# Performance work log

Measured on AMD Instinct MI355X. Metric: run time of the kernel, lower is better.

Reference implementation:

```python
import jax, jax.numpy as jnp
import numpy as np

B, T, D = 32, 1024, 768
H = 768          # GRU hidden size
INNER = 512      # fc output size
NOUT = 39        # out_proj outputs (13 classes x 3 ACCDOA coords)


def setup_inputs() -> dict:
    key = jax.random.key(0)
    ks = jax.random.split(key, 16)
    s_in = 1.0 / np.sqrt(H)
    inp = {
        "features": jax.random.normal(ks[0], (B, T, D), jnp.float32),
        "padding_mask": jnp.zeros((B, T), jnp.bool_),
        # GRU layer 0 (input D -> H), PyTorch gate order [r, z, n]
        "w_ih0": jax.random.uniform(ks[1], (3 * H, D), jnp.float32, -s_in, s_in),
        "w_hh0": jax.random.uniform(ks[2], (3 * H, H), jnp.float32, -s_in, s_in),
        "b_ih0": jax.random.uniform(ks[3], (3 * H,), jnp.float32, -s_in, s_in),
        "b_hh0": jax.random.uniform(ks[4], (3 * H,), jnp.float32, -s_in, s_in),
        # GRU layer 1 (H -> H)
        "w_ih1": jax.random.uniform(ks[5], (3 * H, H), jnp.float32, -s_in, s_in),
        "w_hh1": jax.random.uniform(ks[6], (3 * H, H), jnp.float32, -s_in, s_in),
        "b_ih1": jax.random.uniform(ks[7], (3 * H,), jnp.float32, -s_in, s_in),
        "b_hh1": jax.random.uniform(ks[8], (3 * H,), jnp.float32, -s_in, s_in),
        # fc: hidden -> inner, then SELU
        "fc_w": jax.random.uniform(ks[9], (INNER, H), jnp.float32, -s_in, s_in),
        "fc_b": jax.random.uniform(ks[10], (INNER,), jnp.float32, -s_in, s_in),
        # out_proj: inner -> num_outs, then tanh
        "out_w": jax.random.uniform(ks[11], (NOUT, INNER), jnp.float32, -1.0 / np.sqrt(INNER), 1.0 / np.sqrt(INNER)),
        "out_b": jax.random.uniform(ks[12], (NOUT,), jnp.float32, -1.0 / np.sqrt(INNER), 1.0 / np.sqrt(INNER)),
    }
    return inp


def _gru_layer(x, w_ih, w_hh, b_ih, b_hh):
    # x: [B, T, Din] -> [B, T, H]; PyTorch GRU math, gate order r,z,n
    b, t, _ = x.shape
    h = w_hh.shape[1]
    # precompute input projections for all timesteps in one big GEMM
    x_proj = jnp.einsum('btd,gd->btg', x, w_ih) + b_ih  # [B, T, 3H]

    def step(h_prev, xp):
        gi_r, gi_z, gi_n = jnp.split(xp, 3, axis=-1)
        gh = h_prev @ w_hh.T + b_hh
        gh_r, gh_z, gh_n = jnp.split(gh, 3, axis=-1)
        r = jax.nn.sigmoid(gi_r + gh_r)
        z = jax.nn.sigmoid(gi_z + gh_z)
        n = jnp.tanh(gi_n + r * gh_n)
        h_new = (1.0 - z) * n + z * h_prev
        return h_new, h_new

    h0 = jnp.zeros((b, h), x.dtype)
    _, ys = jax.lax.scan(step, h0, jnp.swapaxes(x_proj, 0, 1))  # ys: [T, B, H]
    return jnp.swapaxes(ys, 0, 1)


def reference(features, padding_mask, w_ih0, w_hh0, b_ih0, b_hh0,
              w_ih1, w_hh1, b_ih1, b_hh1, fc_w, fc_b, out_w, out_b):
    # dropout_input p=0.0 -> identity (eval); padding_mask unused by forward math
    x = _gru_layer(features, w_ih0, w_hh0, b_ih0, b_hh0)
    x = _gru_layer(x, w_ih1, w_hh1, b_ih1, b_hh1)
    x = jax.nn.selu(x @ fc_w.T + fc_b)          # fc + activation_fn='selu'
    x = jnp.tanh(x @ out_w.T + out_b)           # out_proj + out_activation 'tanh'
    return x
```

## Files before the change

kernel.cpp:

```cpp
#include <hip/hip_runtime.h>
#include <cstdint>

typedef float vf2 __attribute__((ext_vector_type(2)));

#define GB_M 128
#define GB_N 64
#define GB_K 16

__global__ __launch_bounds__(256) void gemm_bt_f32(
    const float* __restrict__ A, const float* __restrict__ B,
    const float* __restrict__ bias, float* __restrict__ C,
    int Mc, int N, int K, int tc_shift, int Tfull, int t0, int act)
{
  __shared__ float As[GB_K][GB_M + 4];
  __shared__ float Bs[GB_K][GB_N + 4];
  const int tid = threadIdx.x;
  const int m0 = blockIdx.y * GB_M;
  const int n0 = blockIdx.x * GB_N;
  const int tx = tid & 15;
  const int ty = tid >> 4;

  const int tcmask = (1 << tc_shift) - 1;
  int arow[2];
#pragma unroll
  for (int i = 0; i < 2; i++) {
    int f = tid + i * 256;
    int row = f >> 2;
    int rc = m0 + row;
    arow[i] = (rc >> tc_shift) * Tfull + t0 + (rc & tcmask);
  }
  const int akq = tid & 3;
  const int brow = tid >> 2;
  const int bn = n0 + brow;

  vf2 acc2[4][4];
#pragma unroll
  for (int i = 0; i < 4; i++)
#pragma unroll
    for (int j = 0; j < 4; j++) acc2[i][j] = (vf2)(0.f);

  for (int k0 = 0; k0 < K; k0 += GB_K) {
#pragma unroll
    for (int i = 0; i < 2; i++) {
      int f = tid + i * 256;
      int row = f >> 2;
      float4 v = *(const float4*)(A + (size_t)arow[i] * K + k0 + akq * 4);
      As[akq * 4 + 0][row] = v.x; As[akq * 4 + 1][row] = v.y;
      As[akq * 4 + 2][row] = v.z; As[akq * 4 + 3][row] = v.w;
    }
    {
      float4 v = make_float4(0.f, 0.f, 0.f, 0.f);
      if (bn < N) v = *(const float4*)(B + (size_t)bn * K + k0 + akq * 4);
      Bs[akq * 4 + 0][brow] = v.x; Bs[akq * 4 + 1][brow] = v.y;
      Bs[akq * 4 + 2][brow] = v.z; Bs[akq * 4 + 3][brow] = v.w;
    }
    __syncthreads();
#pragma unroll
    for (int k = 0; k < GB_K; k++) {
      float4 a0 = *(const float4*)&As[k][ty * 8];
      float4 a1 = *(const float4*)&As[k][ty * 8 + 4];
      float4 b0 = *(const float4*)&Bs[k][tx * 4];
      vf2 a2[4];
      a2[0] = (vf2){a0.x, a0.y}; a2[1] = (vf2){a0.z, a0.w};
      a2[2] = (vf2){a1.x, a1.y}; a2[3] = (vf2){a1.z, a1.w};
      float bv[4] = {b0.x, b0.y, b0.z, b0.w};
#pragma unroll
      for (int j = 0; j < 4; j++) {
        vf2 bs = (vf2){bv[j], bv[j]};
#pragma unroll
        for (int ip = 0; ip < 4; ip++)
          acc2[ip][j] = __builtin_elementwise_fma(a2[ip], bs, acc2[ip][j]);
      }
    }
    __syncthreads();
  }

#pragma unroll
  for (int j = 0; j < 4; j++) {
    int n = n0 + tx * 4 + j;
    if (n >= N) continue;
    float bz = bias[n];
#pragma unroll
    for (int i = 0; i < 8; i++) {
      int m = m0 + ty * 8 + i;
      float x = ((i & 1) ? acc2[i >> 1][j].y : acc2[i >> 1][j].x) + bz;
      if (act == 1) {
        x = 1.0507009873554805f * (x > 0.f ? x : 1.6732632423543772f * (__expf(x) - 1.f));
      } else if (act == 2) {
        x = tanhf(x);
      }
      C[(size_t)m * N + n] = x;
    }
  }
}

#define RT 384
#define RNWG 256

__device__ __forceinline__ void pollge(const unsigned* fp, unsigned want) {
  while (__hip_atomic_load(fp, __ATOMIC_RELAXED, __HIP_MEMORY_SCOPE_AGENT) < want)
    __builtin_amdgcn_s_sleep(1);
}

__global__ __launch_bounds__(RT, 1) void gru_rec(
    const float* __restrict__ gi, const float* __restrict__ w_hh,
    const float* __restrict__ b_hh, float* __restrict__ hb,
    unsigned* __restrict__ flags, float* __restrict__ seq,
    int t0, int Tc)
{
  __shared__ float hs[8][776];
  const int wg = blockIdx.x;
  const int jg = wg & 63;
  const int sd = wg >> 6;
  const int j0 = jg * 12;
  const int tid = threadIdx.x;
  const int p  = tid >> 6;
  const int ks = tid & 63;

  unsigned* flagX_my = flags + (((0 * 4 + sd) * 64) + jg) * 16;
  unsigned* flagY_my = flags + (((1 * 4 + sd) * 64) + jg) * 16;

  float4 wreg[3][2][3];
#pragma unroll
  for (int g = 0; g < 3; g++)
#pragma unroll
    for (int j2 = 0; j2 < 2; j2++)
#pragma unroll
      for (int kk = 0; kk < 3; kk++)
        wreg[g][j2][kk] = *(const float4*)(
            w_hh + (size_t)(g * 768 + j0 + 2 * p + j2) * 768 + (kk * 64 + ks) * 4);

  const int j2l = (ks >> 2) & 1;
  const int cl  = ks & 3;
  const int j_out  = j0 + 2 * p + j2l;
  const int bX_out = 8 * sd + cl;
  const int bY_out = 8 * sd + 4 + cl;
  const float bhr = b_hh[j_out];
  const float bhz = b_hh[768 + j_out];
  const float bhn = b_hh[1536 + j_out];

  const int sbi = tid / 96;
  const int sk  = tid - sbi * 96;
  const int jgA = (sk * 8) / 12;
  const int jgB = (sk * 8 + 7) / 12;
  const unsigned* fXA = flags + ((0 * 4 + sd) * 64 + jgA) * 16;
  const unsigned* fXB = flags + ((0 * 4 + sd) * 64 + jgB) * 16;
  const unsigned* fYA = flags + ((1 * 4 + sd) * 64 + jgA) * 16;
  const unsigned* fYB = flags + ((1 * 4 + sd) * 64 + jgB) * 16;

  const bool hi4 = (ks & 4) != 0;
  const bool hi2 = (ks & 2) != 0;
  const bool hi1 = (ks & 1) != 0;

  for (int tt = 0; tt < Tc; tt++) {
    const int t = t0 + tt;

    pollge(fXA, (unsigned)t);
    pollge(fXB, (unsigned)t);
    {
      const unsigned long long* src = (const unsigned long long*)
          (hb + (size_t)(t & 1) * 24576 + (size_t)(8 * sd + sbi) * 768) + sk * 4;
      unsigned long long v[4];
#pragma unroll
      for (int i = 0; i < 4; i++)
        v[i] = __hip_atomic_load(src + i, __ATOMIC_RELAXED, __HIP_MEMORY_SCOPE_AGENT);
      float* dst = &hs[sbi][sk * 8];
      *(float4*)dst = make_float4(
          __uint_as_float((unsigned)v[0]), __uint_as_float((unsigned)(v[0] >> 32)),
          __uint_as_float((unsigned)v[1]), __uint_as_float((unsigned)(v[1] >> 32)));
      *(float4*)(dst + 4) = make_float4(
          __uint_as_float((unsigned)v[2]), __uint_as_float((unsigned)(v[2] >> 32)),
          __uint_as_float((unsigned)v[3]), __uint_as_float((unsigned)(v[3] >> 32)));
    }
    float gXr = 0.f, gXz = 0.f, gXn = 0.f;
    if (ks < 8) {
      const float* gX = gi + ((size_t)bX_out * Tc + tt) * 2304 + j_out;
      gXr = gX[0]; gXz = gX[768]; gXn = gX[1536];
    }
    __syncthreads();
    if (tid == 0)
      __hip_atomic_store(flagY_my, (unsigned)t, __ATOMIC_RELAXED, __HIP_MEMORY_SCOPE_AGENT);

    float r3[3];
    {
      vf2 a2[3][2][4];
#pragma unroll
      for (int g = 0; g < 3; g++)
#pragma unroll
        for (int j2 = 0; j2 < 2; j2++)
#pragma unroll
          for (int c = 0; c < 4; c++) a2[g][j2][c] = (vf2)(0.f);
#pragma unroll
      for (int kk = 0; kk < 3; kk++) {
        const int off = (kk * 64 + ks) * 4;
        vf2 hlo[4], hhi[4];
#pragma unroll
        for (int c = 0; c < 4; c++) {
          float4 h = *(const float4*)(&hs[c][0] + off);
          hlo[c] = (vf2){h.x, h.y};
          hhi[c] = (vf2){h.z, h.w};
        }
#pragma unroll
        for (int g = 0; g < 3; g++)
#pragma unroll
          for (int j2 = 0; j2 < 2; j2++) {
            float4 w = wreg[g][j2][kk];
            vf2 wlo = (vf2){w.x, w.y};
            vf2 whi = (vf2){w.z, w.w};
#pragma unroll
            for (int c = 0; c < 4; c++) {
              a2[g][j2][c] = __builtin_elementwise_fma(wlo, hlo[c], a2[g][j2][c]);
              a2[g][j2][c] = __builtin_elementwise_fma(whi, hhi[c], a2[g][j2][c]);
            }
          }
      }
      float acc[3][2][4];
#pragma unroll
      for (int g = 0; g < 3; g++)
#pragma unroll
        for (int j2 = 0; j2 < 2; j2++)
#pragma unroll
          for (int c = 0; c < 4; c++) acc[g][j2][c] = a2[g][j2][c].x + a2[g][j2][c].y;

      float r12[3][4];
#pragma unroll
      for (int g = 0; g < 3; g++)
#pragma unroll
        for (int c = 0; c < 4; c++) {
          float send = hi4 ? acc[g][0][c] : acc[g][1][c];
          float keep = hi4 ? acc[g][1][c] : acc[g][0][c];
          r12[g][c] = keep + __shfl_xor(send, 4);
        }
      float r6[3][2];
#pragma unroll
      for (int g = 0; g < 3; g++)
#pragma unroll
        for (int c2 = 0; c2 < 2; c2++) {
          float send = hi2 ? r12[g][c2] : r12[g][2 + c2];
          float keep = hi2 ? r12[g][2 + c2] : r12[g][c2];
          r6[g][c2] = keep + __shfl_xor(send, 2);
        }
#pragma unroll
      for (int g = 0; g < 3; g++) {
        float send = hi1 ? r6[g][0] : r6[g][1];
        float keep = hi1 ? r6[g][1] : r6[g][0];
        r3[g] = keep + __shfl_xor(send, 1);
      }
#pragma unroll
      for (int g = 0; g < 3; g++) {
        r3[g] += __shfl_xor(r3[g], 8);
        r3[g] += __shfl_xor(r3[g], 16);
        r3[g] += __shfl_xor(r3[g], 32);
      }
    }
    if (ks < 8) {
      float hp = hs[cl][j_out];
      float r = 1.f / (1.f + __expf(-(gXr + r3[0] + bhr)));
      float z = 1.f / (1.f + __expf(-(gXz + r3[1] + bhz)));
      float n = tanhf(gXn + r * (r3[2] + bhn));
      float hv = (1.f - z) * n + z * hp;
      __hip_atomic_store(hb + (size_t)((t + 1) & 1) * 24576 + (size_t)bX_out * 768 + j_out,
                         hv, __ATOMIC_RELAXED, __HIP_MEMORY_SCOPE_AGENT);
      seq[((size_t)bX_out * 1024 + t) * 768 + j_out] = hv;
    }

    pollge(fYA, (unsigned)t);
    pollge(fYB, (unsigned)t);
    {
      const unsigned long long* src = (const unsigned long long*)
          (hb + (size_t)(t & 1) * 24576 + (size_t)(8 * sd + 4 + sbi) * 768) + sk * 4;
      unsigned long long v[4];
#pragma unroll
      for (int i = 0; i < 4; i++)
        v[i] = __hip_atomic_load(src + i, __ATOMIC_RELAXED, __HIP_MEMORY_SCOPE_AGENT);
      float* dst = &hs[4 + sbi][sk * 8];
      *(float4*)dst = make_float4(
          __uint_as_float((unsigned)v[0]), __uint_as_float((unsigned)(v[0] >> 32)),
          __uint_as_float((unsigned)v[1]), __uint_as_float((unsigned)(v[1] >> 32)));
      *(float4*)(dst + 4) = make_float4(
          __uint_as_float((unsigned)v[2]), __uint_as_float((unsigned)(v[2] >> 32)),
          __uint_as_float((unsigned)v[3]), __uint_as_float((unsigned)(v[3] >> 32)));
    }
    float gYr = 0.f, gYz = 0.f, gYn = 0.f;
    if (ks < 8) {
      const float* gY = gi + ((size_t)bY_out * Tc + tt) * 2304 + j_out;
      gYr = gY[0]; gYz = gY[768]; gYn = gY[1536];
    }
    __syncthreads();
    if (tid == 0)
      __hip_atomic_store(flagX_my, (unsigned)(t + 1), __ATOMIC_RELAXED, __HIP_MEMORY_SCOPE_AGENT);

    {
      vf2 a2[3][2][4];
#pragma unroll
      for (int g = 0; g < 3; g++)
#pragma unroll
        for (int j2 = 0; j2 < 2; j2++)
#pragma unroll
          for (int c = 0; c < 4; c++) a2[g][j2][c] = (vf2)(0.f);
#pragma unroll
      for (int kk = 0; kk < 3; kk++) {
        const int off = (kk * 64 + ks) * 4;
        vf2 hlo[4], hhi[4];
#pragma unroll
        for (int c = 0; c < 4; c++) {
          float4 h = *(const float4*)(&hs[4 + c][0] + off);
          hlo[c] = (vf2){h.x, h.y};
          hhi[c] = (vf2){h.z, h.w};
        }
#pragma unroll
        for (int g = 0; g < 3; g++)
#pragma unroll
          for (int j2 = 0; j2 < 2; j2++) {
            float4 w = wreg[g][j2][kk];
            vf2 wlo = (vf2){w.x, w.y};
            vf2 whi = (vf2){w.z, w.w};
#pragma unroll
            for (int c = 0; c < 4; c++) {
              a2[g][j2][c] = __builtin_elementwise_fma(wlo, hlo[c], a2[g][j2][c]);
              a2[g][j2][c] = __builtin_elementwise_fma(whi, hhi[c], a2[g][j2][c]);
            }
          }
      }
      float acc[3][2][4];
#pragma unroll
      for (int g = 0; g < 3; g++)
#pragma unroll
        for (int j2 = 0; j2 < 2; j2++)
#pragma unroll
          for (int c = 0; c < 4; c++) acc[g][j2][c] = a2[g][j2][c].x + a2[g][j2][c].y;

      float r12[3][4];
#pragma unroll
      for (int g = 0; g < 3; g++)
#pragma unroll
        for (int c = 0; c < 4; c++) {
          float send = hi4 ? acc[g][0][c] : acc[g][1][c];
          float keep = hi4 ? acc[g][1][c] : acc[g][0][c];
          r12[g][c] = keep + __shfl_xor(send, 4);
        }
      float r6[3][2];
#pragma unroll
      for (int g = 0; g < 3; g++)
#pragma unroll
        for (int c2 = 0; c2 < 2; c2++) {
          float send = hi2 ? r12[g][c2] : r12[g][2 + c2];
          float keep = hi2 ? r12[g][2 + c2] : r12[g][c2];
          r6[g][c2] = keep + __shfl_xor(send, 2);
        }
#pragma unroll
      for (int g = 0; g < 3; g++) {
        float send = hi1 ? r6[g][0] : r6[g][1];
        float keep = hi1 ? r6[g][1] : r6[g][0];
        r3[g] = keep + __shfl_xor(send, 1);
      }
#pragma unroll
      for (int g = 0; g < 3; g++) {
        r3[g] += __shfl_xor(r3[g], 8);
        r3[g] += __shfl_xor(r3[g], 16);
        r3[g] += __shfl_xor(r3[g], 32);
      }
    }
    if (ks < 8) {
      float hp = hs[4 + cl][j_out];
      float r = 1.f / (1.f + __expf(-(gYr + r3[0] + bhr)));
      float z = 1.f / (1.f + __expf(-(gYz + r3[1] + bhz)));
      float n = tanhf(gYn + r * (r3[2] + bhn));
      float hv = (1.f - z) * n + z * hp;
      __hip_atomic_store(hb + (size_t)((t + 1) & 1) * 24576 + (size_t)bY_out * 768 + j_out,
                         hv, __ATOMIC_RELAXED, __HIP_MEMORY_SCOPE_AGENT);
      seq[((size_t)bY_out * 1024 + t) * 768 + j_out] = hv;
    }
  }
  __syncthreads();
  if (tid == 0)
    __hip_atomic_store(flagY_my, (unsigned)(t0 + Tc), __ATOMIC_RELAXED, __HIP_MEMORY_SCOPE_AGENT);
}

extern "C" void kernel_launch(void* const* d_in, const int* in_sizes, int n_in,
                              void* d_out, int out_size, void* d_ws, size_t ws_size,
                              hipStream_t stream) {
  const float* feat  = (const float*)d_in[0];
  const float* w_ih0 = (const float*)d_in[2];
  const float* w_hh0 = (const float*)d_in[3];
  const float* b_ih0 = (const float*)d_in[4];
  const float* b_hh0 = (const float*)d_in[5];
  const float* w_ih1 = (const float*)d_in[6];
  const float* w_hh1 = (const float*)d_in[7];
  const float* b_ih1 = (const float*)d_in[8];
  const float* b_hh1 = (const float*)d_in[9];
  const float* fc_w  = (const float*)d_in[10];
  const float* fc_b  = (const float*)d_in[11];
  const float* out_w = (const float*)d_in[12];
  const float* out_b = (const float*)d_in[13];
  float* out = (float*)d_out;

  const int Tc = 256;
  const int McChunk = 32 * Tc;
  const size_t DYN_LDS = 65536;

  float* proj = (float*)d_ws;
  float* seq  = proj + (size_t)32 * Tc * 2304;
  float* hbuf = seq + (size_t)25165824;
  unsigned* flags = (unsigned*)(hbuf + 2 * 24576);

  hipMemsetAsync(hbuf, 0, 2 * 24576 * sizeof(float), stream);
  hipMemsetAsync(flags, 0, 32768, stream);
  for (int c = 0; c < 4; c++) {
    gemm_bt_f32<<<dim3(36, McChunk / 128), dim3(256), 0, stream>>>(
        feat, w_ih0, b_ih0, proj, McChunk, 2304, 768, 8, 1024, c * Tc, 0);
    gru_rec<<<dim3(RNWG), dim3(RT), DYN_LDS, stream>>>(
        proj, w_hh0, b_hh0, hbuf, flags, seq, c * Tc, Tc);
  }
  hipMemsetAsync(hbuf, 0, 2 * 24576 * sizeof(float), stream);
  hipMemsetAsync(flags, 0, 32768, stream);
  for (int c = 0; c < 4; c++) {
    gemm_bt_f32<<<dim3(36, McChunk / 128), dim3(256), 0, stream>>>(
        seq, w_ih1, b_ih1, proj, McChunk, 2304, 768, 8, 1024, c * Tc, 0);
    gru_rec<<<dim3(RNWG), dim3(RT), DYN_LDS, stream>>>(
        proj, w_hh1, b_hh1, hbuf, flags, seq, c * Tc, Tc);
  }
  gemm_bt_f32<<<dim3(8, 256), dim3(256), 0, stream>>>(
      seq, fc_w, fc_b, proj, 32768, 512, 768, 15, 32768, 0, 1);
  gemm_bt_f32<<<dim3(1, 256), dim3(256), 0, stream>>>(
      proj, out_w, out_b, out, 32768, 39, 512, 15, 32768, 0, 2);
}
```

Measured before the change: 14.04 ms.

## Merge two half-batch recurrence phases into one sync per timestep

The GRU recurrence kernel now does one flag poll and one gather of all 8 batch rows of h per timestep, instead of two staggered half-batch phases each with its own flags, poll and barrier. The gi loads for both halves are issued before polling so their latency is hidden, and the dynamic LDS reservation is dropped. This halves the number of cross-workgroup handshakes per step but removes the overlap the X/Y split gave, where one half's matvec could run while the other half's h was still arriving.

```diff
diff --git a/kernel.cpp b/kernel.cpp
--- a/kernel.cpp
+++ b/kernel.cpp
@@ -117,8 +117,7 @@
   const int p  = tid >> 6;
   const int ks = tid & 63;
 
-  unsigned* flagX_my = flags + (((0 * 4 + sd) * 64) + jg) * 16;
-  unsigned* flagY_my = flags + (((1 * 4 + sd) * 64) + jg) * 16;
+  unsigned* flag_my = flags + ((size_t)(sd * 64) + jg) * 16;
 
   float4 wreg[3][2][3];
 #pragma unroll
@@ -132,21 +131,17 @@
 
   const int j2l = (ks >> 2) & 1;
   const int cl  = ks & 3;
-  const int j_out  = j0 + 2 * p + j2l;
-  const int bX_out = 8 * sd + cl;
-  const int bY_out = 8 * sd + 4 + cl;
+  const int j_out = j0 + 2 * p + j2l;
+  const int bA = 8 * sd + cl;
+  const int bB = 8 * sd + 4 + cl;
   const float bhr = b_hh[j_out];
   const float bhz = b_hh[768 + j_out];
   const float bhn = b_hh[1536 + j_out];
 
-  const int sbi = tid / 96;
-  const int sk  = tid - sbi * 96;
-  const int jgA = (sk * 8) / 12;
-  const int jgB = (sk * 8 + 7) / 12;
-  const unsigned* fXA = flags + ((0 * 4 + sd) * 64 + jgA) * 16;
-  const unsigned* fXB = flags + ((0 * 4 + sd) * 64 + jgB) * 16;
-  const unsigned* fYA = flags + ((1 * 4 + sd) * 64 + jgA) * 16;
-  const unsigned* fYB = flags + ((1 * 4 + sd) * 64 + jgB) * 16;
+  const int sbi = tid >> 5;
+  const int sk  = tid & 31;
+  const unsigned* f0 = flags + ((size_t)(sd * 64) + 2 * sk) * 16;
+  const unsigned* f1 = flags + ((size_t)(sd * 64) + 2 * sk + 1) * 16;
 
   const bool hi4 = (ks & 4) != 0;
   const bool hi2 = (ks & 2) != 0;
@@ -155,33 +150,37 @@
   for (int tt = 0; tt < Tc; tt++) {
     const int t = t0 + tt;
 
-    pollge(fXA, (unsigned)t);
-    pollge(fXB, (unsigned)t);
-    {
+    float gAr = 0.f, gAz = 0.f, gAn = 0.f;
+    float gBr = 0.f, gBz = 0.f, gBn = 0.f;
+    if (ks < 8) {
+      const float* gA = gi + ((size_t)bA * Tc + tt) * 2304 + j_out;
+      gAr = gA[0]; gAz = gA[768]; gAn = gA[1536];
+      const float* gB = gi + ((size_t)bB * Tc + tt) * 2304 + j_out;
+      gBr = gB[0]; gBz = gB[768]; gBn = gB[1536];
+    }
+
+    if (tid < 256) {
+      pollge(f0, (unsigned)t);
+      pollge(f1, (unsigned)t);
       const unsigned long long* src = (const unsigned long long*)
-          (hb + (size_t)(t & 1) * 24576 + (size_t)(8 * sd + sbi) * 768) + sk * 4;
-      unsigned long long v[4];
-#pragma unroll
-      for (int i = 0; i < 4; i++)
+          (hb + (size_t)(t & 1) * 24576 + (size_t)(8 * sd + sbi) * 768) + sk * 12;
+      unsigned long long v[12];
+#pragma unroll
+      for (int i = 0; i < 12; i++)
         v[i] = __hip_atomic_load(src + i, __ATOMIC_RELAXED, __HIP_MEMORY_SCOPE_AGENT);
-      float* dst = &hs[sbi][sk * 8];
-      *(float4*)dst = make_float4(
-          __uint_as_float((unsigned)v[0]), __uint_as_float((unsigned)(v[0] >> 32)),
-          __uint_as_float((unsigned)v[1]), __uint_as_float((unsigned)(v[1] >> 32)));
-      *(float4*)(dst + 4) = make_float4(
-          __uint_as_float((unsigned)v[2]), __uint_as_float((unsigned)(v[2] >> 32)),
-          __uint_as_float((unsigned)v[3]), __uint_as_float((unsigned)(v[3] >> 32)));
-    }
-    float gXr = 0.f, gXz = 0.f, gXn = 0.f;
-    if (ks < 8) {
-      const float* gX = gi + ((size_t)bX_out * Tc + tt) * 2304 + j_out;
-      gXr = gX[0]; gXz = gX[768]; gXn = gX[1536];
+      float* dst = &hs[sbi][sk * 24];
+#pragma unroll
+      for (int q = 0; q < 6; q++) {
+        *(float4*)(dst + q * 4) = make_float4(
+            __uint_as_float((unsigned)v[2 * q]),
+            __uint_as_float((unsigned)(v[2 * q] >> 32)),
+            __uint_as_float((unsigned)v[2 * q + 1]),
+            __uint_as_float((unsigned)(v[2 * q + 1] >> 32)));
+      }
     }
     __syncthreads();
-    if (tid == 0)
-      __hip_atomic_store(flagY_my, (unsigned)t, __ATOMIC_RELAXED, __HIP_MEMORY_SCOPE_AGENT);
-
-    float r3[3];
+
+    float rA[3];
     {
       vf2 a2[3][2][4];
 #pragma unroll
@@ -244,52 +243,17 @@
       for (int g = 0; g < 3; g++) {
         float send = hi1 ? r6[g][0] : r6[g][1];
         float keep = hi1 ? r6[g][1] : r6[g][0];
-        r3[g] = keep + __shfl_xor(send, 1);
+        rA[g] = keep + __shfl_xor(send, 1);
       }
 #pragma unroll
       for (int g = 0; g < 3; g++) {
-        r3[g] += __shfl_xor(r3[g], 8);
-        r3[g] += __shfl_xor(r3[g], 16);
-        r3[g] += __shfl_xor(r3[g], 32);
-      }
-    }
-    if (ks < 8) {
-      float hp = hs[cl][j_out];
-      float r = 1.f / (1.f + __expf(-(gXr + r3[0] + bhr)));
-      float z = 1.f / (1.f + __expf(-(gXz + r3[1] + bhz)));
-      float n = tanhf(gXn + r * (r3[2] + bhn));
-      float hv = (1.f - z) * n + z * hp;
-      __hip_atomic_store(hb + (size_t)((t + 1) & 1) * 24576 + (size_t)bX_out * 768 + j_out,
-                         hv, __ATOMIC_RELAXED, __HIP_MEMORY_SCOPE_AGENT);
-      seq[((size_t)bX_out * 1024 + t) * 768 + j_out] = hv;
-    }
-
-    pollge(fYA, (unsigned)t);
-    pollge(fYB, (unsigned)t);
-    {
-      const unsigned long long* src = (const unsigned long long*)
-          (hb + (size_t)(t & 1) * 24576 + (size_t)(8 * sd + 4 + sbi) * 768) + sk * 4;
-      unsigned long long v[4];
-#pragma unroll
-      for (int i = 0; i < 4; i++)
-        v[i] = __hip_atomic_load(src + i, __ATOMIC_RELAXED, __HIP_MEMORY_SCOPE_AGENT);
-      float* dst = &hs[4 + sbi][sk * 8];
-      *(float4*)dst = make_float4(
-          __uint_as_float((unsigned)v[0]), __uint_as_float((unsigned)(v[0] >> 32)),
-          __uint_as_float((unsigned)v[1]), __uint_as_float((unsigned)(v[1] >> 32)));
-      *(float4*)(dst + 4) = make_float4(
-          __uint_as_float((unsigned)v[2]), __uint_as_float((unsigned)(v[2] >> 32)),
-          __uint_as_float((unsigned)v[3]), __uint_as_float((unsigned)(v[3] >> 32)));
-    }
-    float gYr = 0.f, gYz = 0.f, gYn = 0.f;
-    if (ks < 8) {
-      const float* gY = gi + ((size_t)bY_out * Tc + tt) * 2304 + j_out;
-      gYr = gY[0]; gYz = gY[768]; gYn = gY[1536];
-    }
-    __syncthreads();
-    if (tid == 0)
-      __hip_atomic_store(flagX_my, (unsigned)(t + 1), __ATOMIC_RELAXED, __HIP_MEMORY_SCOPE_AGENT);
-
+        rA[g] += __shfl_xor(rA[g], 8);
+        rA[g] += __shfl_xor(rA[g], 16);
+        rA[g] += __shfl_xor(rA[g], 32);
+      }
+    }
+
+    float rB[3];
     {
       vf2 a2[3][2][4];
 #pragma unroll
@@ -352,29 +316,42 @@
       for (int g = 0; g < 3; g++) {
         float send = hi1 ? r6[g][0] : r6[g][1];
         float keep = hi1 ? r6[g][1] : r6[g][0];
-        r3[g] = keep + __shfl_xor(send, 1);
+        rB[g] = keep + __shfl_xor(send, 1);
       }
 #pragma unroll
       for (int g = 0; g < 3; g++) {
-        r3[g] += __shfl_xor(r3[g], 8);
-        r3[g] += __shfl_xor(r3[g], 16);
-        r3[g] += __shfl_xor(r3[g], 32);
-      }
-    }
+        rB[g] += __shfl_xor(rB[g], 8);
+        rB[g] += __shfl_xor(rB[g], 16);
+        rB[g] += __shfl_xor(rB[g], 32);
+      }
+    }
+
     if (ks < 8) {
-      float hp = hs[4 + cl][j_out];
-      float r = 1.f / (1.f + __expf(-(gYr + r3[0] + bhr)));
-      float z = 1.f / (1.f + __expf(-(gYz + r3[1] + bhz)));
-      float n = tanhf(gYn + r * (r3[2] + bhn));
-      float hv = (1.f - z) * n + z * hp;
-      __hip_atomic_store(hb + (size_t)((t + 1) & 1) * 24576 + (size_t)bY_out * 768 + j_out,
-                         hv, __ATOMIC_RELAXED, __HIP_MEMORY_SCOPE_AGENT);
-      seq[((size_t)bY_out * 1024 + t) * 768 + j_out] = hv;
-    }
-  }
-  __syncthreads();
-  if (tid == 0)
-    __hip_atomic_store(flagY_my, (unsigned)(t0 + Tc), __ATOMIC_RELAXED, __HIP_MEMORY_SCOPE_AGENT);
+      {
+        float hp = hs[cl][j_out];
+        float r = 1.f / (1.f + __expf(-(gAr + rA[0] + bhr)));
+        float z = 1.f / (1.f + __expf(-(gAz + rA[1] + bhz)));
+        float n = tanhf(gAn + r * (rA[2] + bhn));
+        float hv = (1.f - z) * n + z * hp;
+        __hip_atomic_store(hb + (size_t)((t + 1) & 1) * 24576 + (size_t)bA * 768 + j_out,
+                           hv, __ATOMIC_RELAXED, __HIP_MEMORY_SCOPE_AGENT);
+        seq[((size_t)bA * 1024 + t) * 768 + j_out] = hv;
+      }
+      {
+        float hp = hs[4 + cl][j_out];
+        float r = 1.f / (1.f + __expf(-(gBr + rB[0] + bhr)));
+        float z = 1.f / (1.f + __expf(-(gBz + rB[1] + bhz)));
+        float n = tanhf(gBn + r * (rB[2] + bhn));
+        float hv = (1.f - z) * n + z * hp;
+        __hip_atomic_store(hb + (size_t)((t + 1) & 1) * 24576 + (size_t)bB * 768 + j_out,
+                           hv, __ATOMIC_RELAXED, __HIP_MEMORY_SCOPE_AGENT);
+        seq[((size_t)bB * 1024 + t) * 768 + j_out] = hv;
+      }
+    }
+    __syncthreads();
+    if (tid == 0)
+      __hip_atomic_store(flag_my, (unsigned)(t + 1), __ATOMIC_RELAXED, __HIP_MEMORY_SCOPE_AGENT);
+  }
 }
 
 extern "C" void kernel_launch(void* const* d_in, const int* in_sizes, int n_in,
@@ -397,7 +374,6 @@
 
   const int Tc = 256;
   const int McChunk = 32 * Tc;
-  const size_t DYN_LDS = 65536;
 
   float* proj = (float*)d_ws;
   float* seq  = proj + (size_t)32 * Tc * 2304;
@@ -409,7 +385,7 @@
   for (int c = 0; c < 4; c++) {
     gemm_bt_f32<<<dim3(36, McChunk / 128), dim3(256), 0, stream>>>(
         feat, w_ih0, b_ih0, proj, McChunk, 2304, 768, 8, 1024, c * Tc, 0);
-    gru_rec<<<dim3(RNWG), dim3(RT), DYN_LDS, stream>>>(
+    gru_rec<<<dim3(RNWG), dim3(RT), 0, stream>>>(
         proj, w_hh0, b_hh0, hbuf, flags, seq, c * Tc, Tc);
   }
   hipMemsetAsync(hbuf, 0, 2 * 24576 * sizeof(float), stream);
@@ -417,7 +393,7 @@
   for (int c = 0; c < 4; c++) {
     gemm_bt_f32<<<dim3(36, McChunk / 128), dim3(256), 0, stream>>>(
         seq, w_ih1, b_ih1, proj, McChunk, 2304, 768, 8, 1024, c * Tc, 0);
-    gru_rec<<<dim3(RNWG), dim3(RT), DYN_LDS, stream>>>(
+    gru_rec<<<dim3(RNWG), dim3(RT), 0, stream>>>(
         proj, w_hh1, b_hh1, hbuf, flags, seq, c * Tc, Tc);
   }
   gemm_bt_f32<<<dim3(8, 256), dim3(256), 0, stream>>>(
```

Result: slower. 16.69 ms (+18.9%).
